# Kernel tuning notes

Measured on AMD Instinct MI355X. Metric: run time of the kernel, lower is better.

The kernel has to match this reference:

```python
import jax, jax.numpy as jnp
import numpy as np

B, N, D = 8, 192, 768   # batch of docs, events per doc, embed_dim
H = 150                 # Score hidden_dim
PAD = -1000.0           # pad_and_stack fill value


def setup_inputs() -> dict:
    key = jax.random.key(0)
    ks = jax.random.split(key, 7)
    s1 = 1.0 / np.sqrt(3 * D)
    s2 = 1.0 / np.sqrt(H)
    return {
        "event_embed": jax.random.normal(ks[0], (B, N, D), jnp.float32),
        "W1": jax.random.normal(ks[1], (3 * D, H), jnp.float32) * s1,
        "b1": jnp.zeros((H,), jnp.float32),
        "W2": jax.random.normal(ks[2], (H, H), jnp.float32) * s2,
        "b2": jnp.zeros((H,), jnp.float32),
        "W3": jax.random.normal(ks[3], (H, 1), jnp.float32) * s2,
        "b3": jnp.zeros((1,), jnp.float32),
    }


def reference(event_embed, W1, b1, W2, b2, W3, b3):
    Bq, Nq, Dq = event_embed.shape
    # antecedent pairs: for each event i, all k < i (row-major, matches torch loop order)
    rows, cols = jnp.tril_indices(Nq, k=-1)          # [P], P = N*(N-1)/2
    i_g = event_embed[:, rows]                        # [B, P, D]
    j_g = event_embed[:, cols]                        # [B, P, D]
    pairs = jnp.concatenate([i_g, j_g, i_g * j_g], axis=-1)  # [B, P, 3D]
    # Score MLP (dropout is identity at inference)
    h = jax.nn.relu(pairs @ W1 + b1)                  # [B, P, H]
    h = jax.nn.relu(h @ W2 + b2)                      # [B, P, H]
    s = (h @ W3 + b3)[..., 0]                         # [B, P]
    # Scatter pair scores into [B, N, N]; diagonal stays 0 = epsilon score.
    logits = jnp.zeros((Bq, Nq, Nq), event_embed.dtype).at[:, rows, cols].set(s)
    tri = jnp.tril(jnp.ones((Nq, Nq), dtype=bool))    # valid cols: k <= i (incl epsilon)
    masked = jnp.where(tri, logits, -jnp.inf)
    probs = jax.nn.softmax(masked, axis=-1)           # ragged softmax per event row
    return jnp.where(tri, probs, jnp.asarray(PAD, probs.dtype))  # pad_and_stack(value=-1000)
```

## Files before the change

### kernel.cpp

```cpp
#include <hip/hip_runtime.h>
#include <hip/hip_bf16.h>

#define NSEQ   192
#define PADV   -1000.0f
#define NEGINF -1.0e30f

typedef __bf16 bf16x8 __attribute__((ext_vector_type(8)));
typedef float  f32x4  __attribute__((ext_vector_type(4)));

__device__ __forceinline__ void glds16(const void* g, void* l) {
  __builtin_amdgcn_global_load_lds(
      (const __attribute__((address_space(1))) unsigned int*)g,
      (__attribute__((address_space(3))) unsigned int*)l, 16, 0, 0);
}

#define MFMA16(a, b, c) __builtin_amdgcn_mfma_f32_16x16x32_bf16((a), (b), (c), 0, 0, 0)

__global__ __launch_bounds__(256) void prep_pack(const float* __restrict__ W1,
                                                 const float* __restrict__ W2,
                                                 const float* __restrict__ b1,
                                                 __bf16* __restrict__ W1abp,
                                                 __bf16* __restrict__ W1cp,
                                                 __bf16* __restrict__ W2p,
                                                 float* __restrict__ b1p) {
  int idx = blockIdx.x * 256 + threadIdx.x;
  if (idx < 245760) {
    int e = idx & 7, l = (idx >> 3) & 63, t = idx >> 9;
    int ct = t % 20, kk = t / 20;
    int k = kk * 32 + ((l >> 4) << 3) + e;
    int hp = ct * 16 + (l & 15);
    int col = (hp < 160) ? hp : hp - 160;
    int rbase = (hp < 160) ? 0 : 768;
    float v = (col < 150) ? W1[(size_t)(rbase + k) * 150 + col] : 0.f;
    W1abp[idx] = (__bf16)v;
  } else if (idx < 393216) {
    int j = idx - 245760;
    int kk = j / 6144, rem = j % 6144;
    int q = rem >> 9, l = (rem >> 3) & 63, e = rem & 7;
    int k = kk * 32 + ((l >> 4) << 3) + e;
    int h = q * 16 + (l & 15);
    float v = (q < 10 && h < 150) ? W1[(size_t)(1536 + k) * 150 + h] : 0.f;
    W1cp[j] = (__bf16)v;
  } else if (idx < 423936) {
    int j = idx - 393216;
    int s = j / 6144, rem = j % 6144;
    int q = rem >> 9, l = (rem >> 3) & 63, e = rem & 7;
    int k = s * 32 + ((l >> 4) << 3) + e;
    int h = q * 16 + (l & 15);
    float v = (q < 10 && k < 150 && h < 150) ? W2[(size_t)k * 150 + h] : 0.f;
    W2p[j] = (__bf16)v;
  } else if (idx < 424096) {
    int h = idx - 423936;
    b1p[h] = (h < 150) ? b1[h] : 0.f;
  }
}

__global__ __launch_bounds__(256) void prep_gemm(const float* __restrict__ E,
                                                 const __bf16* __restrict__ W1abp,
                                                 float* __restrict__ A12) {
  int tid = threadIdx.x;
  int w = tid >> 6, l = tid & 63, m = l & 15, kg = l >> 4;
  int mt = blockIdx.x >> 3;
  int c  = blockIdx.x & 7;
  const float* ep = E + (size_t)(mt * 16 + m) * 768 + c * 96;

  f32x4 acc[5];
#pragma unroll
  for (int u = 0; u < 5; ++u) acc[u] = (f32x4){0.f, 0.f, 0.f, 0.f};

#pragma unroll
  for (int kk = 0; kk < 3; ++kk) {
    int k = kk * 32 + kg * 8;
    f32x4 x0 = *(const f32x4*)(ep + k);
    f32x4 x1 = *(const f32x4*)(ep + k + 4);
    bf16x8 af;
#pragma unroll
    for (int e = 0; e < 4; ++e) { af[e] = (__bf16)x0[e]; af[e + 4] = (__bf16)x1[e]; }
    const bf16x8* wp = (const bf16x8*)W1abp + (size_t)(((c * 3 + kk) * 20) + w * 5) * 64 + l;
#pragma unroll
    for (int u = 0; u < 5; ++u)
      acc[u] = MFMA16(af, wp[u * 64], acc[u]);
  }
#pragma unroll
  for (int u = 0; u < 5; ++u)
#pragma unroll
    for (int r = 0; r < 4; ++r)
      atomicAdd(&A12[(size_t)(mt * 16 + kg * 4 + r) * 320 + (w * 5 + u) * 16 + m], acc[u][r]);
}

__global__ __launch_bounds__(512, 4) void pair_mlp(
    const float* __restrict__ E, const float* __restrict__ A12,
    const __bf16* __restrict__ W1cp, const __bf16* __restrict__ W2p,
    const float* __restrict__ b1p, const float* __restrict__ b2,
    const float* __restrict__ W3, const float* __restrict__ b3,
    float* __restrict__ out) {
  __shared__ alignas(16) char pool[75648];
  char* eib = pool + 24576;
  char* ejb = pool + 49152;

  const int tid = threadIdx.x;
  const int w = tid >> 6, l = tid & 63;
  const int m = l & 15, kg = l >> 4;
  const int jr0 = 2 * w, jr1 = 2 * w + 1;

  int bid = blockIdx.x;
  int blk = (bid & 7) * 78 + (bid >> 3);
  int b = blk / 78, r0 = blk - b * 78;
  int it = (int)((sqrtf(8.f * (float)r0 + 1.f) - 1.f) * 0.5f);
  while (it * (it + 1) / 2 > r0) --it;
  while ((it + 1) * (it + 2) / 2 <= r0) ++it;
  int jt = r0 - it * (it + 1) / 2;

  const int ibase = b * NSEQ + it * 16;
  const int jbase = b * NSEQ + jt * 16;

  if (w < 6) {
#pragma unroll
    for (int q = 0; q < 2; ++q)
      glds16(W1cp + (size_t)(2 * w + q) * 512 + l * 8,
             pool + (2 * w + q) * 1024 + l * 16);
  }

#pragma unroll
  for (int q = 0; q < 3; ++q) {
    int t = tid + 512 * q;
    int r = t / 96, d = t - (t / 96) * 96;
    int sc = d ^ (r & 7);
    const float* si = E + (size_t)(ibase + r) * 768 + sc * 8;
    const float* sj = E + (size_t)(jbase + r) * 768 + sc * 8;
    f32x4 a0 = *(const f32x4*)(si);
    f32x4 a1 = *(const f32x4*)(si + 4);
    f32x4 c0 = *(const f32x4*)(sj);
    f32x4 c1 = *(const f32x4*)(sj + 4);
    bf16x8 vi, vj;
#pragma unroll
    for (int e = 0; e < 4; ++e) {
      vi[e] = (__bf16)a0[e]; vi[e + 4] = (__bf16)a1[e];
      vj[e] = (__bf16)c0[e]; vj[e + 4] = (__bf16)c1[e];
    }
    *(bf16x8*)(eib + r * 1536 + d * 16) = vi;
    *(bf16x8*)(ejb + r * 1536 + d * 16) = vj;
  }

  if (tid < 160) {
    float* bwf = (float*)(pool + 73728);
    bwf[tid]       = (tid < 150) ? b2[tid] : 0.f;
    bwf[160 + tid] = (tid < 150) ? W3[tid] : 0.f;
  }
  float b3v = b3[0];

  f32x4 acc1[10][2];
#pragma unroll
  for (int ct = 0; ct < 10; ++ct) {
    f32x4 a1v = *(const f32x4*)(A12 + (size_t)(ibase + m) * 320 + ct * 16 + kg * 4);
    f32x4 b1v = *(const f32x4*)(b1p + ct * 16 + kg * 4);
#pragma unroll
    for (int pt = 0; pt < 2; ++pt) {
      f32x4 a2v = *(const f32x4*)(A12 + (size_t)(jbase + jr0 + pt) * 320 + 160 + ct * 16 + kg * 4);
      acc1[ct][pt] = a1v + a2v + b1v;
    }
  }

  __syncthreads();

  auto compute = [&](int kk) {
    const __bf16* wb = (const __bf16*)(pool + (kk & 1) * 12288);
    int cb = kk * 4 + kg;
    bf16x8 eiv = *(const bf16x8*)(eib + m * 1536 + ((cb ^ (m & 7)) << 4));
    bf16x8 ej0 = *(const bf16x8*)(ejb + jr0 * 1536 + ((cb ^ (jr0 & 7)) << 4));
    bf16x8 ej1 = *(const bf16x8*)(ejb + jr1 * 1536 + ((cb ^ (jr1 & 7)) << 4));
    bf16x8 pf0, pf1;
#pragma unroll
    for (int e = 0; e < 8; ++e) {
      float ei = (float)eiv[e];
      pf0[e] = (__bf16)(ei * (float)ej0[e]);
      pf1[e] = (__bf16)(ei * (float)ej1[e]);
    }
    __builtin_amdgcn_s_setprio(1);
#pragma unroll
    for (int ct = 0; ct < 10; ++ct) {
      bf16x8 wf = *(const bf16x8*)(wb + ct * 512 + l * 8);
      acc1[ct][0] = MFMA16(wf, pf0, acc1[ct][0]);
      acc1[ct][1] = MFMA16(wf, pf1, acc1[ct][1]);
    }
    __builtin_amdgcn_s_setprio(0);
  };

  for (int kk = 0; kk < 23; ++kk) {
    if (w < 6) {
#pragma unroll
      for (int q = 0; q < 2; ++q)
        glds16(W1cp + ((size_t)(kk + 1) * 12 + 2 * w + q) * 512 + l * 8,
               pool + ((kk + 1) & 1) * 12288 + (2 * w + q) * 1024 + l * 16);
      asm volatile("s_waitcnt vmcnt(2)" ::: "memory");
    }
    __builtin_amdgcn_s_barrier();
    compute(kk);
    __builtin_amdgcn_s_barrier();
  }
  if (w < 6) asm volatile("s_waitcnt vmcnt(0)" ::: "memory");
  __builtin_amdgcn_s_barrier();
  compute(23);
  __builtin_amdgcn_s_barrier();

  char* hb = pool + 24576 + w * 6144;
  auto write_h1 = [&](int p) {
#pragma unroll
    for (int ct = 0; ct < 10; ++ct) {
      union { __bf16 h[4]; unsigned u[2]; } cv;
      cv.h[0] = (__bf16)fmaxf(acc1[ct][p][0], 0.f);
      cv.h[1] = (__bf16)fmaxf(acc1[ct][p][1], 0.f);
      cv.h[2] = (__bf16)fmaxf(acc1[ct][p][2], 0.f);
      cv.h[3] = (__bf16)fmaxf(acc1[ct][p][3], 0.f);
      int c = (2 * ct + (kg >> 1)) ^ (m & 7);
      char* dst = hb + m * 384 + c * 16 + (kg & 1) * 8;
      *(unsigned*)(dst)     = cv.u[0];
      *(unsigned*)(dst + 4) = cv.u[1];
    }
  };
  write_h1(0);
  if (w < 6) {
#pragma unroll
    for (int q = 0; q < 2; ++q)
      glds16(W2p + (size_t)(2 * w + q) * 512 + l * 8,
             pool + (2 * w + q) * 1024 + l * 16);
  }

  const float* bwp = (const float*)(pool + 73728);
  f32x4 acc2[10];
#pragma unroll
  for (int ct = 0; ct < 10; ++ct) acc2[ct] = (f32x4){0.f, 0.f, 0.f, 0.f};

  for (int rr = 0; rr < 10; ++rr) {
    int p = rr / 5, s = rr - p * 5;
    if (rr == 5) write_h1(1);
    if (rr < 9) {
      int ns = (rr + 1 >= 5) ? rr + 1 - 5 : rr + 1;
      if (w < 6) {
#pragma unroll
        for (int q = 0; q < 2; ++q)
          glds16(W2p + ((size_t)ns * 12 + 2 * w + q) * 512 + l * 8,
                 pool + ((rr + 1) & 1) * 12288 + (2 * w + q) * 1024 + l * 16);
        asm volatile("s_waitcnt vmcnt(2)" ::: "memory");
      }
    } else {
      if (w < 6) asm volatile("s_waitcnt vmcnt(0)" ::: "memory");
    }
    __builtin_amdgcn_s_barrier();

    const __bf16* wb2 = (const __bf16*)(pool + (rr & 1) * 12288);
    bf16x8 af = *(const bf16x8*)(hb + m * 384 + (((4 * s + kg) ^ (m & 7)) << 4));
    __builtin_amdgcn_s_setprio(1);
#pragma unroll
    for (int ct = 0; ct < 10; ++ct) {
      bf16x8 wf = *(const bf16x8*)(wb2 + ct * 512 + l * 8);
      acc2[ct] = MFMA16(wf, af, acc2[ct]);
    }
    __builtin_amdgcn_s_setprio(0);

    if (s == 4) {
      float sum = 0.f;
#pragma unroll
      for (int ct = 0; ct < 10; ++ct) {
        f32x4 b2q = *(const f32x4*)(bwp + ct * 16 + kg * 4);
        f32x4 w3q = *(const f32x4*)(bwp + 160 + ct * 16 + kg * 4);
#pragma unroll
        for (int r = 0; r < 4; ++r)
          sum += fmaxf(acc2[ct][r] + b2q[r], 0.f) * w3q[r];
      }
      sum += __shfl_xor(sum, 16, 64);
      sum += __shfl_xor(sum, 32, 64);
      if (kg == 0) {
        int il = it * 16 + m;
        int jl = jt * 16 + 2 * w + p;
        if (jl < il)
          out[(size_t)(b * NSEQ + il) * NSEQ + jl] = sum + b3v;
      }
#pragma unroll
      for (int ct = 0; ct < 10; ++ct) acc2[ct] = (f32x4){0.f, 0.f, 0.f, 0.f};
    }
    __builtin_amdgcn_s_barrier();
  }
}

__global__ __launch_bounds__(256) void softmax_rows(float* __restrict__ out) {
  int w = threadIdx.x >> 6, l = threadIdx.x & 63;
  int blk = blockIdx.x * 4 + w;
  int i = blk % NSEQ;
  size_t base = (size_t)blk * NSEQ;
  float v[3];
  float mx = NEGINF;
#pragma unroll
  for (int t = 0; t < 3; ++t) {
    int j = l + 64 * t;
    float x = (j < i) ? out[base + j] : (j == i ? 0.f : NEGINF);
    v[t] = x;
    mx = fmaxf(mx, x);
  }
#pragma unroll
  for (int off = 32; off >= 1; off >>= 1) mx = fmaxf(mx, __shfl_xor(mx, off, 64));
  float s = 0.f;
#pragma unroll
  for (int t = 0; t < 3; ++t) s += __expf(v[t] - mx);
#pragma unroll
  for (int off = 32; off >= 1; off >>= 1) s += __shfl_xor(s, off, 64);
  float inv = 1.0f / s;
#pragma unroll
  for (int t = 0; t < 3; ++t) {
    int j = l + 64 * t;
    out[base + j] = (j <= i) ? __expf(v[t] - mx) * inv : PADV;
  }
}

extern "C" void kernel_launch(void* const* d_in, const int* in_sizes, int n_in,
                              void* d_out, int out_size, void* d_ws, size_t ws_size,
                              hipStream_t stream) {
  const float* E  = (const float*)d_in[0];
  const float* W1 = (const float*)d_in[1];
  const float* b1 = (const float*)d_in[2];
  const float* W2 = (const float*)d_in[3];
  const float* b2 = (const float*)d_in[4];
  const float* W3 = (const float*)d_in[5];
  const float* b3 = (const float*)d_in[6];
  float* out = (float*)d_out;

  char* ws = (char*)d_ws;
  float*  A12   = (float*)(ws);
  __bf16* W1abp = (__bf16*)(ws + 1966080);
  __bf16* W1cp  = (__bf16*)(ws + 2457600);
  __bf16* W2p   = (__bf16*)(ws + 2752512);
  float*  b1p   = (float*)(ws + 2813952);

  hipMemsetAsync(A12, 0, 1966080, stream);
  prep_pack<<<1657, 256, 0, stream>>>(W1, W2, b1, W1abp, W1cp, W2p, b1p);
  prep_gemm<<<768, 256, 0, stream>>>(E, W1abp, A12);
  pair_mlp<<<624, 512, 0, stream>>>(E, A12, W1cp, W2p, b1p, b2, W3, b3, out);
  softmax_rows<<<384, 256, 0, stream>>>(out);
}
```

Before: 100.3 us.

## Split pair_mlp into 16x8 tiles with 4 waves and a unified triple-buffered pipeline

Halves the block size to 256 threads and tiles pairs as 16 i-rows by 8 j-rows, which doubles the grid to 1248 blocks and lets the tile enumeration skip more of the upper triangle. The W1c and W2 weight chunks now stream through a single 34-step loop with a three-slot LDS ring. That allows one barrier per step instead of two, and the first-layer to second-layer transition no longer drains the pipeline. Each wave loads three chunks so all waves share the copy work. The cost is that each block reloads all weights for half as many pairs, roughly doubling weight traffic from L2, and each block does more barriers relative to its MFMA work.

```diff
diff --git a/kernel.cpp b/kernel.cpp
--- a/kernel.cpp
+++ b/kernel.cpp
@@ -88,15 +88,15 @@
       atomicAdd(&A12[(size_t)(mt * 16 + kg * 4 + r) * 320 + (w * 5 + u) * 16 + m], acc[u][r]);
 }
 
-__global__ __launch_bounds__(512, 4) void pair_mlp(
+__global__ __launch_bounds__(256) void pair_mlp(
     const float* __restrict__ E, const float* __restrict__ A12,
     const __bf16* __restrict__ W1cp, const __bf16* __restrict__ W2p,
     const float* __restrict__ b1p, const float* __restrict__ b2,
     const float* __restrict__ W3, const float* __restrict__ b3,
     float* __restrict__ out) {
   __shared__ alignas(16) char pool[75648];
-  char* eib = pool + 24576;
-  char* ejb = pool + 49152;
+  char* eib = pool + 36864;
+  char* ejb = pool + 61440;
 
   const int tid = threadIdx.x;
   const int w = tid >> 6, l = tid & 63;
@@ -104,42 +104,37 @@
   const int jr0 = 2 * w, jr1 = 2 * w + 1;
 
   int bid = blockIdx.x;
-  int blk = (bid & 7) * 78 + (bid >> 3);
-  int b = blk / 78, r0 = blk - b * 78;
-  int it = (int)((sqrtf(8.f * (float)r0 + 1.f) - 1.f) * 0.5f);
-  while (it * (it + 1) / 2 > r0) --it;
-  while ((it + 1) * (it + 2) / 2 <= r0) ++it;
-  int jt = r0 - it * (it + 1) / 2;
+  int blk = (bid & 7) * 156 + (bid >> 3);
+  int b = blk / 156, r0 = blk - b * 156;
+  int it = (int)((sqrtf(4.f * (float)r0 + 1.f) - 1.f) * 0.5f);
+  while (it * it + it > r0) --it;
+  while ((it + 1) * (it + 1) + (it + 1) <= r0) ++it;
+  int jt = r0 - it * it - it;
 
   const int ibase = b * NSEQ + it * 16;
-  const int jbase = b * NSEQ + jt * 16;
-
-  if (w < 6) {
-#pragma unroll
-    for (int q = 0; q < 2; ++q)
-      glds16(W1cp + (size_t)(2 * w + q) * 512 + l * 8,
-             pool + (2 * w + q) * 1024 + l * 16);
-  }
-
-#pragma unroll
-  for (int q = 0; q < 3; ++q) {
-    int t = tid + 512 * q;
-    int r = t / 96, d = t - (t / 96) * 96;
+  const int jbase = b * NSEQ + jt * 8;
+
+  {
+    const __bf16* src = W1cp + (size_t)(w * 3) * 512;
+    char* dst = pool + (w * 3) * 1024;
+#pragma unroll
+    for (int q = 0; q < 3; ++q) glds16(src + q * 512 + l * 8, dst + q * 1024);
+  }
+
+#pragma unroll
+  for (int q = 0; q < 9; ++q) {
+    int t = tid + 256 * q;
+    int isI = (t < 1536);
+    int tt = isI ? t : t - 1536;
+    int r = tt / 96, d = tt - (tt / 96) * 96;
     int sc = d ^ (r & 7);
-    const float* si = E + (size_t)(ibase + r) * 768 + sc * 8;
-    const float* sj = E + (size_t)(jbase + r) * 768 + sc * 8;
-    f32x4 a0 = *(const f32x4*)(si);
-    f32x4 a1 = *(const f32x4*)(si + 4);
-    f32x4 c0 = *(const f32x4*)(sj);
-    f32x4 c1 = *(const f32x4*)(sj + 4);
-    bf16x8 vi, vj;
-#pragma unroll
-    for (int e = 0; e < 4; ++e) {
-      vi[e] = (__bf16)a0[e]; vi[e + 4] = (__bf16)a1[e];
-      vj[e] = (__bf16)c0[e]; vj[e + 4] = (__bf16)c1[e];
-    }
-    *(bf16x8*)(eib + r * 1536 + d * 16) = vi;
-    *(bf16x8*)(ejb + r * 1536 + d * 16) = vj;
+    const float* src = E + (size_t)((isI ? ibase : jbase) + r) * 768 + sc * 8;
+    f32x4 a0 = *(const f32x4*)(src);
+    f32x4 a1 = *(const f32x4*)(src + 4);
+    bf16x8 v;
+#pragma unroll
+    for (int e = 0; e < 4; ++e) { v[e] = (__bf16)a0[e]; v[e + 4] = (__bf16)a1[e]; }
+    *(bf16x8*)((isI ? eib : ejb) + r * 1536 + d * 16) = v;
   }
 
   if (tid < 160) {
@@ -163,47 +158,9 @@
 
   __syncthreads();
 
-  auto compute = [&](int kk) {
-    const __bf16* wb = (const __bf16*)(pool + (kk & 1) * 12288);
-    int cb = kk * 4 + kg;
-    bf16x8 eiv = *(const bf16x8*)(eib + m * 1536 + ((cb ^ (m & 7)) << 4));
-    bf16x8 ej0 = *(const bf16x8*)(ejb + jr0 * 1536 + ((cb ^ (jr0 & 7)) << 4));
-    bf16x8 ej1 = *(const bf16x8*)(ejb + jr1 * 1536 + ((cb ^ (jr1 & 7)) << 4));
-    bf16x8 pf0, pf1;
-#pragma unroll
-    for (int e = 0; e < 8; ++e) {
-      float ei = (float)eiv[e];
-      pf0[e] = (__bf16)(ei * (float)ej0[e]);
-      pf1[e] = (__bf16)(ei * (float)ej1[e]);
-    }
-    __builtin_amdgcn_s_setprio(1);
-#pragma unroll
-    for (int ct = 0; ct < 10; ++ct) {
-      bf16x8 wf = *(const bf16x8*)(wb + ct * 512 + l * 8);
-      acc1[ct][0] = MFMA16(wf, pf0, acc1[ct][0]);
-      acc1[ct][1] = MFMA16(wf, pf1, acc1[ct][1]);
-    }
-    __builtin_amdgcn_s_setprio(0);
-  };
-
-  for (int kk = 0; kk < 23; ++kk) {
-    if (w < 6) {
-#pragma unroll
-      for (int q = 0; q < 2; ++q)
-        glds16(W1cp + ((size_t)(kk + 1) * 12 + 2 * w + q) * 512 + l * 8,
-               pool + ((kk + 1) & 1) * 12288 + (2 * w + q) * 1024 + l * 16);
-      asm volatile("s_waitcnt vmcnt(2)" ::: "memory");
-    }
-    __builtin_amdgcn_s_barrier();
-    compute(kk);
-    __builtin_amdgcn_s_barrier();
-  }
-  if (w < 6) asm volatile("s_waitcnt vmcnt(0)" ::: "memory");
-  __builtin_amdgcn_s_barrier();
-  compute(23);
-  __builtin_amdgcn_s_barrier();
-
-  char* hb = pool + 24576 + w * 6144;
+  char* hb = pool + 36864 + w * 6144;
+  f32x4 acc2[10];
+
   auto write_h1 = [&](int p) {
 #pragma unroll
     for (int ct = 0; ct < 10; ++ct) {
@@ -218,68 +175,84 @@
       *(unsigned*)(dst + 4) = cv.u[1];
     }
   };
-  write_h1(0);
-  if (w < 6) {
-#pragma unroll
-    for (int q = 0; q < 2; ++q)
-      glds16(W2p + (size_t)(2 * w + q) * 512 + l * 8,
-             pool + (2 * w + q) * 1024 + l * 16);
-  }
 
   const float* bwp = (const float*)(pool + 73728);
-  f32x4 acc2[10];
-#pragma unroll
-  for (int ct = 0; ct < 10; ++ct) acc2[ct] = (f32x4){0.f, 0.f, 0.f, 0.f};
-
-  for (int rr = 0; rr < 10; ++rr) {
-    int p = rr / 5, s = rr - p * 5;
-    if (rr == 5) write_h1(1);
-    if (rr < 9) {
-      int ns = (rr + 1 >= 5) ? rr + 1 - 5 : rr + 1;
-      if (w < 6) {
-#pragma unroll
-        for (int q = 0; q < 2; ++q)
-          glds16(W2p + ((size_t)ns * 12 + 2 * w + q) * 512 + l * 8,
-                 pool + ((rr + 1) & 1) * 12288 + (2 * w + q) * 1024 + l * 16);
-        asm volatile("s_waitcnt vmcnt(2)" ::: "memory");
-      }
+
+  for (int t = 0; t < 34; ++t) {
+    if (t < 33) {
+      int tn = t + 1;
+      const __bf16* src = (tn < 24)
+          ? (W1cp + ((size_t)tn * 12 + w * 3) * 512)
+          : (W2p + ((size_t)((tn - 24) % 5) * 12 + w * 3) * 512);
+      char* dst = pool + (tn % 3) * 12288 + (w * 3) * 1024;
+#pragma unroll
+      for (int q = 0; q < 3; ++q) glds16(src + q * 512 + l * 8, dst + q * 1024);
+      asm volatile("s_waitcnt vmcnt(3)" ::: "memory");
     } else {
-      if (w < 6) asm volatile("s_waitcnt vmcnt(0)" ::: "memory");
+      asm volatile("s_waitcnt vmcnt(0)" ::: "memory");
     }
     __builtin_amdgcn_s_barrier();
 
-    const __bf16* wb2 = (const __bf16*)(pool + (rr & 1) * 12288);
-    bf16x8 af = *(const bf16x8*)(hb + m * 384 + (((4 * s + kg) ^ (m & 7)) << 4));
-    __builtin_amdgcn_s_setprio(1);
-#pragma unroll
-    for (int ct = 0; ct < 10; ++ct) {
-      bf16x8 wf = *(const bf16x8*)(wb2 + ct * 512 + l * 8);
-      acc2[ct] = MFMA16(wf, af, acc2[ct]);
+    const __bf16* wb = (const __bf16*)(pool + (t % 3) * 12288);
+
+    if (t < 24) {
+      int cb = t * 4 + kg;
+      bf16x8 eiv = *(const bf16x8*)(eib + m * 1536 + ((cb ^ (m & 7)) << 4));
+      bf16x8 ej0 = *(const bf16x8*)(ejb + jr0 * 1536 + ((cb ^ (jr0 & 7)) << 4));
+      bf16x8 ej1 = *(const bf16x8*)(ejb + jr1 * 1536 + ((cb ^ (jr1 & 7)) << 4));
+      bf16x8 pf0, pf1;
+#pragma unroll
+      for (int e = 0; e < 8; ++e) {
+        float ei = (float)eiv[e];
+        pf0[e] = (__bf16)(ei * (float)ej0[e]);
+        pf1[e] = (__bf16)(ei * (float)ej1[e]);
+      }
+      __builtin_amdgcn_s_setprio(1);
+#pragma unroll
+      for (int ct = 0; ct < 10; ++ct) {
+        bf16x8 wf = *(const bf16x8*)(wb + ct * 512 + l * 8);
+        acc1[ct][0] = MFMA16(wf, pf0, acc1[ct][0]);
+        acc1[ct][1] = MFMA16(wf, pf1, acc1[ct][1]);
+      }
+      __builtin_amdgcn_s_setprio(0);
+    } else {
+      int r = t - 24;
+      int p = (r >= 5) ? 1 : 0;
+      int s = r - p * 5;
+      if (s == 0) {
+        write_h1(p);
+#pragma unroll
+        for (int ct = 0; ct < 10; ++ct) acc2[ct] = (f32x4){0.f, 0.f, 0.f, 0.f};
+      }
+      bf16x8 af = *(const bf16x8*)(hb + m * 384 + (((4 * s + kg) ^ (m & 7)) << 4));
+      __builtin_amdgcn_s_setprio(1);
+#pragma unroll
+      for (int ct = 0; ct < 10; ++ct) {
+        bf16x8 wf = *(const bf16x8*)(wb + ct * 512 + l * 8);
+        acc2[ct] = MFMA16(wf, af, acc2[ct]);
+      }
+      __builtin_amdgcn_s_setprio(0);
+
+      if (s == 4) {
+        float sum = 0.f;
+#pragma unroll
+        for (int ct = 0; ct < 10; ++ct) {
+          f32x4 b2q = *(const f32x4*)(bwp + ct * 16 + kg * 4);
+          f32x4 w3q = *(const f32x4*)(bwp + 160 + ct * 16 + kg * 4);
+#pragma unroll
+          for (int r2 = 0; r2 < 4; ++r2)
+            sum += fmaxf(acc2[ct][r2] + b2q[r2], 0.f) * w3q[r2];
+        }
+        sum += __shfl_xor(sum, 16, 64);
+        sum += __shfl_xor(sum, 32, 64);
+        if (kg == 0) {
+          int il = it * 16 + m;
+          int jl = jt * 8 + 2 * w + p;
+          if (jl < il)
+            out[(size_t)(b * NSEQ + il) * NSEQ + jl] = sum + b3v;
+        }
+      }
     }
-    __builtin_amdgcn_s_setprio(0);
-
-    if (s == 4) {
-      float sum = 0.f;
-#pragma unroll
-      for (int ct = 0; ct < 10; ++ct) {
-        f32x4 b2q = *(const f32x4*)(bwp + ct * 16 + kg * 4);
-        f32x4 w3q = *(const f32x4*)(bwp + 160 + ct * 16 + kg * 4);
-#pragma unroll
-        for (int r = 0; r < 4; ++r)
-          sum += fmaxf(acc2[ct][r] + b2q[r], 0.f) * w3q[r];
-      }
-      sum += __shfl_xor(sum, 16, 64);
-      sum += __shfl_xor(sum, 32, 64);
-      if (kg == 0) {
-        int il = it * 16 + m;
-        int jl = jt * 16 + 2 * w + p;
-        if (jl < il)
-          out[(size_t)(b * NSEQ + il) * NSEQ + jl] = sum + b3v;
-      }
-#pragma unroll
-      for (int ct = 0; ct < 10; ++ct) acc2[ct] = (f32x4){0.f, 0.f, 0.f, 0.f};
-    }
-    __builtin_amdgcn_s_barrier();
   }
 }
 
@@ -334,6 +307,6 @@
   hipMemsetAsync(A12, 0, 1966080, stream);
   prep_pack<<<1657, 256, 0, stream>>>(W1, W2, b1, W1abp, W1cp, W2p, b1p);
   prep_gemm<<<768, 256, 0, stream>>>(E, W1abp, A12);
-  pair_mlp<<<624, 512, 0, stream>>>(E, A12, W1cp, W2p, b1p, b2, W3, b3, out);
+  pair_mlp<<<1248, 256, 0, stream>>>(E, A12, W1cp, W2p, b1p, b2, W3, b3, out);
   softmax_rows<<<384, 256, 0, stream>>>(out);
 }
```

Result: slower. 188.7 us (+88.1%).
